# Kernel optimization log

Hardware: AMD Instinct MI355X
Metric: run time of the kernel (lower is better)

## Reference

```python
import jax, jax.numpy as jnp
import numpy as np

B, N, C = 64, 320, 768
H = 12
D = C // H  # 64 head dim


def setup_inputs() -> dict:
    key = jax.random.key(0)
    k1, k2, k3, k4, k5 = jax.random.split(key, 5)
    s = 0.02
    return {
        "x": jax.random.normal(k1, (B, N, C), jnp.float32),
        "w_qkv": jax.random.normal(k2, (3 * C, C), jnp.float32) * s,
        "b_qkv": jax.random.normal(k3, (3 * C,), jnp.float32) * s,
        "w_proj": jax.random.normal(k4, (C, C), jnp.float32) * s,
        "b_proj": jax.random.normal(k5, (C,), jnp.float32) * s,
        "num_t": 64,
        "num_s": 256,
    }


def reference(x, w_qkv, b_qkv, w_proj, b_proj, num_t, num_s):
    Bx, Nx, Cx = x.shape
    scale = 1.0 / jnp.sqrt(jnp.asarray(D, x.dtype))
    # qkv projection: [B,N,3C] -> [3,B,H,N,D]
    qkv = x @ w_qkv.T + b_qkv
    qkv = qkv.reshape(Bx, Nx, 3, H, D).transpose(2, 0, 3, 1, 4)
    q, k, v = qkv[0], qkv[1], qkv[2]
    q_t, q_s = q[:, :, :num_t], q[:, :, num_t:]
    k_t = k[:, :, :num_t]
    v_t = v[:, :, :num_t]
    # template self-attention: [B,H,num_t,num_t]
    attn_t = jax.nn.softmax(jnp.einsum("bhqd,bhkd->bhqk", q_t, k_t) * scale, axis=-1)
    x_t = jnp.einsum("bhqk,bhkd->bhqd", attn_t, v_t)
    x_t = x_t.transpose(0, 2, 1, 3).reshape(Bx, num_t, Cx)
    # search attends to all tokens: [B,H,num_s,N]
    attn_s = jax.nn.softmax(jnp.einsum("bhqd,bhkd->bhqk", q_s, k) * scale, axis=-1)
    x_s = jnp.einsum("bhqk,bhkd->bhqd", attn_s, v)
    x_s = x_s.transpose(0, 2, 1, 3).reshape(Bx, num_s, Cx)
    out = jnp.concatenate([x_t, x_s], axis=1)
    return out @ w_proj.T + b_proj
```

## Files before the change

### kernel.cpp

```cpp
#include <hip/hip_runtime.h>
#include <hip/hip_bf16.h>


typedef __attribute__((ext_vector_type(8))) short short8;
typedef __attribute__((ext_vector_type(4))) float f32x4;
typedef __hip_bfloat16 bf16;

#define NTOK 320
#define CDIM 768
#define NHEAD 12
#define MFMA16(a,b,c) __builtin_amdgcn_mfma_f32_16x16x32_bf16((a),(b),(c),0,0,0)

__device__ __forceinline__ unsigned short bfbits(float v) {
    bf16 h = __float2bfloat16(v);
    unsigned short u; __builtin_memcpy(&u, &h, 2);
    return u;
}

__device__ __forceinline__ short8 ldfrag(const bf16* p) { return *(const short8*)p; }
__device__ __forceinline__ short8 ldfrag(const float* p) {
    float4 a = *(const float4*)p;
    float4 b = *(const float4*)(p + 4);
    short8 r;
    r[0]=(short)bfbits(a.x); r[1]=(short)bfbits(a.y); r[2]=(short)bfbits(a.z); r[3]=(short)bfbits(a.w);
    r[4]=(short)bfbits(b.x); r[5]=(short)bfbits(b.y); r[6]=(short)bfbits(b.z); r[7]=(short)bfbits(b.w);
    return r;
}

__device__ __forceinline__ void stage16(const bf16* g, bf16* l) {
    __builtin_amdgcn_global_load_lds(
        (const __attribute__((address_space(1))) void*)g,
        (__attribute__((address_space(3))) void*)l, 16, 0, 0);
}

__global__ __launch_bounds__(256) void cvt_bf16_kernel(const float* __restrict__ src,
                                                       bf16* __restrict__ dst, int n8)
{
    int i = blockIdx.x * 256 + threadIdx.x;
    const int stride = gridDim.x * 256;
    for (; i < n8; i += stride) {
        const float4 a = ((const float4*)src)[2 * (size_t)i];
        const float4 b = ((const float4*)src)[2 * (size_t)i + 1];
        short8 r;
        r[0]=(short)bfbits(a.x); r[1]=(short)bfbits(a.y); r[2]=(short)bfbits(a.z); r[3]=(short)bfbits(a.w);
        r[4]=(short)bfbits(b.x); r[5]=(short)bfbits(b.y); r[6]=(short)bfbits(b.z); r[7]=(short)bfbits(b.w);
        ((short8*)dst)[i] = r;
    }
}

template<int NOUT, int EPI, int BF16B>
__global__ __launch_bounds__(256) void gemm_bt16(const bf16* __restrict__ A,
                                                 const void* __restrict__ Bmv,
                                                 const float* __restrict__ bias,
                                                 void* __restrict__ o0,
                                                 void* __restrict__ o1,
                                                 void* __restrict__ o2)
{
    __shared__ alignas(16) bf16 As[128 * 32];
    __shared__ alignas(16) bf16 Bs[128 * 32];
    const int tid  = threadIdx.x;
    const int lane = tid & 63;
    const int wv   = tid >> 6;
    const int r16  = lane & 15;
    const int kg   = lane >> 4;

    constexpr int GX  = NOUT / 128;
    constexpr int NWG = GX * 160;
    int flat = blockIdx.y * GX + blockIdx.x;
    flat = (flat & 7) * (NWG >> 3) + (flat >> 3);
    const int byy = flat / GX;
    const int bxx = flat - byy * GX;
    const int m0  = byy * 128;
    const int n0  = bxx * 128;
    const int wm  = (wv & 1) * 64;
    const int wn  = (wv >> 1) * 64;

    const bf16*  Ab   = A + (size_t)m0 * CDIM;
    const bf16*  Bb16 = (const bf16*)Bmv  + (size_t)n0 * CDIM;
    const float* Bb32 = (const float*)Bmv + (size_t)n0 * CDIM;

    const int ra0 = tid >> 2;
    const int ca0 = (tid & 3) * 8;

    bf16* lA0 = &As[(size_t)(wv * 64) * 8];
    bf16* lA1 = &As[(size_t)(wv * 64 + 256) * 8];
    bf16* lB0 = &Bs[(size_t)(wv * 64) * 8];
    bf16* lB1 = &Bs[(size_t)(wv * 64 + 256) * 8];

    f32x4 acc[4][4] = {};

    for (int k0 = 0; k0 < CDIM; k0 += 32) {
        if constexpr (BF16B) {
            __syncthreads();
            stage16(Ab   + (size_t)ra0        * CDIM + k0 + ca0, lA0);
            stage16(Ab   + (size_t)(ra0 + 64) * CDIM + k0 + ca0, lA1);
            stage16(Bb16 + (size_t)ra0        * CDIM + k0 + ca0, lB0);
            stage16(Bb16 + (size_t)(ra0 + 64) * CDIM + k0 + ca0, lB1);
            __syncthreads();
        } else {
            short8 gb0 = ldfrag(Bb32 + (size_t)ra0        * CDIM + k0 + ca0);
            short8 gb1 = ldfrag(Bb32 + (size_t)(ra0 + 64) * CDIM + k0 + ca0);
            __syncthreads();
            stage16(Ab + (size_t)ra0        * CDIM + k0 + ca0, lA0);
            stage16(Ab + (size_t)(ra0 + 64) * CDIM + k0 + ca0, lA1);
            *(short8*)&Bs[(size_t)tid * 8]         = gb0;
            *(short8*)&Bs[(size_t)(tid + 256) * 8] = gb1;
            __syncthreads();
        }

        short8 af[4], bfr[4];
        #pragma unroll
        for (int mt = 0; mt < 4; mt++)
            af[mt] = *(const short8*)&As[(wm + mt * 16 + r16) * 32 + kg * 8];
        #pragma unroll
        for (int nt = 0; nt < 4; nt++)
            bfr[nt] = *(const short8*)&Bs[(wn + nt * 16 + r16) * 32 + kg * 8];
        #pragma unroll
        for (int mt = 0; mt < 4; mt++)
            #pragma unroll
            for (int nt = 0; nt < 4; nt++)
                acc[mt][nt] = MFMA16(af[mt], bfr[nt], acc[mt][nt]);
    }

    #pragma unroll
    for (int nt = 0; nt < 4; nt++) {
        const int gn = n0 + wn + nt * 16 + r16;
        const float bv = bias[gn];
        if (EPI == 0) {
            const int which = gn / CDIM;
            const int rem   = gn - which * CDIM;
            const int hh    = rem >> 6;
            const int dd    = rem & 63;
            #pragma unroll
            for (int mt = 0; mt < 4; mt++) {
                const int gm0  = m0 + wm + mt * 16 + kg * 4;
                const int bidx = gm0 / NTOK;
                const int nn0  = gm0 - bidx * NTOK;
                float v[4];
                #pragma unroll
                for (int r = 0; r < 4; r++) v[r] = acc[mt][nt][r] + bv;
                if (which == 0) {
                    bf16* q = (bf16*)o0 + ((size_t)(bidx * NHEAD + hh) * NTOK + nn0) * 64 + dd;
                    #pragma unroll
                    for (int r = 0; r < 4; r++) q[(size_t)r * 64] = __float2bfloat16(v[r]);
                } else if (which == 1) {
                    bf16* k = (bf16*)o1 + ((size_t)(bidx * NHEAD + hh) * NTOK + nn0) * 64 + dd;
                    #pragma unroll
                    for (int r = 0; r < 4; r++) k[(size_t)r * 64] = __float2bfloat16(v[r]);
                } else {
                    ushort4 p;
                    unsigned short* ps = (unsigned short*)&p;
                    #pragma unroll
                    for (int r = 0; r < 4; r++) ps[r] = bfbits(v[r]);
                    *(ushort4*)((bf16*)o2 + ((size_t)(bidx * NHEAD + hh) * 64 + dd) * NTOK + nn0) = p;
                }
            }
        } else {
            float* out = (float*)o0;
            #pragma unroll
            for (int mt = 0; mt < 4; mt++) {
                const int gm0 = m0 + wm + mt * 16 + kg * 4;
                #pragma unroll
                for (int r = 0; r < 4; r++)
                    out[(size_t)(gm0 + r) * NOUT + gn] = acc[mt][nt][r] + bv;
            }
        }
    }
}

#define SW 324
__global__ __launch_bounds__(256) void attn_kernel(const bf16* __restrict__ q_ws,
                                                   const bf16* __restrict__ k_ws,
                                                   const bf16* __restrict__ vt_ws,
                                                   bf16* __restrict__ attn,
                                                   const int* __restrict__ numt_p)
{
    __shared__ alignas(16) float S[32 * SW];
    __shared__ float rowstat[32];
    int num_t = 64;
    if (numt_p) {
        int v = *numt_p;
        float f = __int_as_float(v);
        if (v >= 1 && v <= 319) num_t = v;
        else if (f >= 1.f && f <= 319.f) num_t = (int)f;
    }
    if (num_t <= 0 || num_t > NTOK || (num_t & 31)) num_t = 64;

    const int tid  = threadIdx.x;
    const int lane = tid & 63;
    const int w    = tid >> 6;
    const int r16  = lane & 15;
    const int kg   = lane >> 4;

    const int blk = blockIdx.x;
    const int bh  = blk / 10;
    const int qt  = blk - bh * 10;
    const int b   = bh / NHEAD;
    const int h   = bh - b * NHEAD;
    const int q0  = qt * 32;
    const int nk  = (q0 + 32 <= num_t) ? num_t : NTOK;
    const int nk16 = nk >> 4;

    const bf16* qp = q_ws  + (size_t)bh * NTOK * 64;
    const bf16* kp = k_ws  + (size_t)bh * NTOK * 64;
    const bf16* vp = vt_ws + (size_t)bh * 64 * NTOK;

    short8 qf[2][2];
    #pragma unroll
    for (int ks = 0; ks < 2; ks++)
        #pragma unroll
        for (int mt = 0; mt < 2; mt++)
            qf[ks][mt] = ldfrag(qp + (size_t)(q0 + mt * 16 + r16) * 64 + ks * 32 + kg * 8);

    const float scale = 0.125f;
    for (int nt = w; nt < nk16; nt += 4) {
        f32x4 a0 = {}, a1 = {};
        #pragma unroll
        for (int ks = 0; ks < 2; ks++) {
            short8 kf = ldfrag(kp + (size_t)(nt * 16 + r16) * 64 + ks * 32 + kg * 8);
            a0 = MFMA16(qf[ks][0], kf, a0);
            a1 = MFMA16(qf[ks][1], kf, a1);
        }
        #pragma unroll
        for (int r = 0; r < 4; r++) {
            S[(kg * 4 + r) * SW + nt * 16 + r16]      = a0[r] * scale;
            S[(16 + kg * 4 + r) * SW + nt * 16 + r16] = a1[r] * scale;
        }
    }
    __syncthreads();

    {
        const int row = tid >> 3;
        const int sub = tid & 7;
        float* Sr = S + row * SW;
        float mx = -1e30f;
        for (int c = sub * 4; c < nk; c += 32) {
            float4 t = *(float4*)&Sr[c];
            mx = fmaxf(mx, fmaxf(fmaxf(t.x, t.y), fmaxf(t.z, t.w)));
        }
        #pragma unroll
        for (int m = 1; m < 8; m <<= 1) mx = fmaxf(mx, __shfl_xor(mx, m));
        float sum = 0.f;
        for (int c = sub * 4; c < nk; c += 32) {
            float4 t = *(float4*)&Sr[c];
            t.x = __expf(t.x - mx); t.y = __expf(t.y - mx);
            t.z = __expf(t.z - mx); t.w = __expf(t.w - mx);
            sum += t.x + t.y + t.z + t.w;
            *(float4*)&Sr[c] = t;
        }
        #pragma unroll
        for (int m = 1; m < 8; m <<= 1) sum += __shfl_xor(sum, m);
        if (sub == 0) rowstat[row] = 1.0f / sum;
    }
    __syncthreads();

    const int mt  = w & 1;
    const int ntb = w >> 1;
    f32x4 o[2] = {};
    for (int ks = 0; ks < (nk >> 5); ks++) {
        const float* pr = &S[(mt * 16 + r16) * SW + ks * 32 + kg * 8];
        short8 af;
        #pragma unroll
        for (int j = 0; j < 8; j++) af[j] = (short)bfbits(pr[j]);
        #pragma unroll
        for (int i = 0; i < 2; i++) {
            const int nt = ntb + i * 2;
            short8 vf = ldfrag(vp + (size_t)(nt * 16 + r16) * NTOK + ks * 32 + kg * 8);
            o[i] = MFMA16(af, vf, o[i]);
        }
    }
    #pragma unroll
    for (int i = 0; i < 2; i++) {
        const int nt = ntb + i * 2;
        const int dd = nt * 16 + r16;
        #pragma unroll
        for (int r = 0; r < 4; r++) {
            const int qrow  = mt * 16 + kg * 4 + r;
            const float val = o[i][r] * rowstat[qrow];
            const int token = q0 + qrow;
            attn[(((size_t)b * NTOK + token) * NHEAD + h) * 64 + dd] = __float2bfloat16(val);
        }
    }
}

extern "C" void kernel_launch(void* const* d_in, const int* in_sizes, int n_in,
                              void* d_out, int out_size, void* d_ws, size_t ws_size,
                              hipStream_t stream)
{
    float* out = (float*)d_out;

    const float *x = nullptr, *w_qkv = nullptr, *b_qkv = nullptr,
                *w_proj = nullptr, *b_proj = nullptr;
    const int* numt_p = nullptr;
    for (int i = 0; i < n_in; i++) {
        switch (in_sizes[i]) {
            case 15728640: x      = (const float*)d_in[i]; break;
            case 1769472:  w_qkv  = (const float*)d_in[i]; break;
            case 2304:     b_qkv  = (const float*)d_in[i]; break;
            case 589824:   w_proj = (const float*)d_in[i]; break;
            case 768:      b_proj = (const float*)d_in[i]; break;
            case 1:        if (!numt_p) numt_p = (const int*)d_in[i]; break;
            default: break;
        }
    }
    if (!x || !w_qkv || !b_qkv || !w_proj || !b_proj) return;

    const size_t per      = (size_t)64 * NHEAD * NTOK * 64;
    const size_t wq_elems = (size_t)2304 * 768;
    const size_t wp_elems = (size_t)768 * 768;
    const size_t base_need = 4 * per * sizeof(bf16);
    const size_t full_need = base_need + (wq_elems + wp_elems) * sizeof(bf16);
    if (ws_size < base_need) return;
    const bool full = ws_size >= full_need;

    bf16* q_ws  = (bf16*)d_ws;
    bf16* k_ws  = q_ws  + per;
    bf16* vt_ws = k_ws  + per;
    bf16* attn  = vt_ws + per;
    bf16* x16   = attn;
    bf16* wq16  = attn + per;
    bf16* wp16  = wq16 + wq_elems;

    cvt_bf16_kernel<<<2048, 256, 0, stream>>>(x, x16, (int)(per / 8));
    if (full) {
        cvt_bf16_kernel<<<864, 256, 0, stream>>>(w_qkv, wq16, (int)(wq_elems / 8));
        cvt_bf16_kernel<<<288, 256, 0, stream>>>(w_proj, wp16, (int)(wp_elems / 8));
    }

    if (full)
        gemm_bt16<2304, 0, 1><<<dim3(18, 160), 256, 0, stream>>>(
            x16, wq16, b_qkv, q_ws, k_ws, vt_ws);
    else
        gemm_bt16<2304, 0, 0><<<dim3(18, 160), 256, 0, stream>>>(
            x16, w_qkv, b_qkv, q_ws, k_ws, vt_ws);

    attn_kernel<<<768 * 10, 256, 0, stream>>>(q_ws, k_ws, vt_ws, attn, numt_p);

    if (full)
        gemm_bt16<768, 1, 1><<<dim3(6, 160), 256, 0, stream>>>(
            attn, wp16, b_proj, out, nullptr, nullptr);
    else
        gemm_bt16<768, 1, 0><<<dim3(6, 160), 256, 0, stream>>>(
            attn, w_proj, b_proj, out, nullptr, nullptr);
}
```

Before: 398.8 us.

## Fuse bf16 conversion launches, remap attention blocks per XCD, store P as bf16

Merges the three fp32-to-bf16 conversion launches into one kernel that walks a concatenated index range, removing two launches. Remaps attention block IDs so that consecutive blocks sharing a batch-head land on the same XCD (blk&7 interleave), which should improve L2 reuse of K/V. After the softmax exp, probabilities are written in place as bf16, so the PV loop loads an MFMA fragment directly instead of converting eight floats per step. In-place aliasing of the bf16 rows inside the float rows relies on each row being handled only by its own threads before the barrier.

```diff
diff --git a/kernel.cpp b/kernel.cpp
--- a/kernel.cpp
+++ b/kernel.cpp
@@ -33,18 +33,24 @@
         (__attribute__((address_space(3))) void*)l, 16, 0, 0);
 }
 
-__global__ __launch_bounds__(256) void cvt_bf16_kernel(const float* __restrict__ src,
-                                                       bf16* __restrict__ dst, int n8)
+__global__ __launch_bounds__(256) void cvt3_kernel(const float* __restrict__ s0, bf16* __restrict__ d0, int n0,
+                                                   const float* __restrict__ s1, bf16* __restrict__ d1, int n1,
+                                                   const float* __restrict__ s2, bf16* __restrict__ d2, int n2)
 {
+    const int ntot = n0 + n1 + n2;
     int i = blockIdx.x * 256 + threadIdx.x;
     const int stride = gridDim.x * 256;
-    for (; i < n8; i += stride) {
-        const float4 a = ((const float4*)src)[2 * (size_t)i];
-        const float4 b = ((const float4*)src)[2 * (size_t)i + 1];
+    for (; i < ntot; i += stride) {
+        const float* s; bf16* d; int j = i;
+        if (j < n0)              { s = s0; d = d0; }
+        else if ((j -= n0) < n1) { s = s1; d = d1; }
+        else                     { j -= n1; s = s2; d = d2; }
+        const float4 a = ((const float4*)s)[2 * (size_t)j];
+        const float4 b = ((const float4*)s)[2 * (size_t)j + 1];
         short8 r;
         r[0]=(short)bfbits(a.x); r[1]=(short)bfbits(a.y); r[2]=(short)bfbits(a.z); r[3]=(short)bfbits(a.w);
         r[4]=(short)bfbits(b.x); r[5]=(short)bfbits(b.y); r[6]=(short)bfbits(b.z); r[7]=(short)bfbits(b.w);
-        ((short8*)dst)[i] = r;
+        ((short8*)d)[j] = r;
     }
 }
 
@@ -169,6 +175,7 @@
 }
 
 #define SW 324
+#define ATTN_NWG (768 * 10)
 __global__ __launch_bounds__(256) void attn_kernel(const bf16* __restrict__ q_ws,
                                                    const bf16* __restrict__ k_ws,
                                                    const bf16* __restrict__ vt_ws,
@@ -192,7 +199,8 @@
     const int r16  = lane & 15;
     const int kg   = lane >> 4;
 
-    const int blk = blockIdx.x;
+    int blk = blockIdx.x;
+    blk = (blk & 7) * (ATTN_NWG / 8) + (blk >> 3);
     const int bh  = blk / 10;
     const int qt  = blk - bh * 10;
     const int b   = bh / NHEAD;
@@ -233,6 +241,7 @@
         const int row = tid >> 3;
         const int sub = tid & 7;
         float* Sr = S + row * SW;
+        bf16*  Pr = (bf16*)Sr;
         float mx = -1e30f;
         for (int c = sub * 4; c < nk; c += 32) {
             float4 t = *(float4*)&Sr[c];
@@ -246,7 +255,9 @@
             t.x = __expf(t.x - mx); t.y = __expf(t.y - mx);
             t.z = __expf(t.z - mx); t.w = __expf(t.w - mx);
             sum += t.x + t.y + t.z + t.w;
-            *(float4*)&Sr[c] = t;
+            ushort4 p;
+            p.x = bfbits(t.x); p.y = bfbits(t.y); p.z = bfbits(t.z); p.w = bfbits(t.w);
+            *(ushort4*)&Pr[c] = p;
         }
         #pragma unroll
         for (int m = 1; m < 8; m <<= 1) sum += __shfl_xor(sum, m);
@@ -256,12 +267,10 @@
 
     const int mt  = w & 1;
     const int ntb = w >> 1;
+    const bf16* Pb = (const bf16*)S;
     f32x4 o[2] = {};
     for (int ks = 0; ks < (nk >> 5); ks++) {
-        const float* pr = &S[(mt * 16 + r16) * SW + ks * 32 + kg * 8];
-        short8 af;
-        #pragma unroll
-        for (int j = 0; j < 8; j++) af[j] = (short)bfbits(pr[j]);
+        short8 af = *(const short8*)&Pb[(size_t)(mt * 16 + r16) * (SW * 2) + ks * 32 + kg * 8];
         #pragma unroll
         for (int i = 0; i < 2; i++) {
             const int nt = ntb + i * 2;
@@ -321,11 +330,13 @@
     bf16* wq16  = attn + per;
     bf16* wp16  = wq16 + wq_elems;
 
-    cvt_bf16_kernel<<<2048, 256, 0, stream>>>(x, x16, (int)(per / 8));
-    if (full) {
-        cvt_bf16_kernel<<<864, 256, 0, stream>>>(w_qkv, wq16, (int)(wq_elems / 8));
-        cvt_bf16_kernel<<<288, 256, 0, stream>>>(w_proj, wp16, (int)(wp_elems / 8));
-    }
+    if (full)
+        cvt3_kernel<<<2048, 256, 0, stream>>>(x, x16, (int)(per / 8),
+                                              w_qkv, wq16, (int)(wq_elems / 8),
+                                              w_proj, wp16, (int)(wp_elems / 8));
+    else
+        cvt3_kernel<<<2048, 256, 0, stream>>>(x, x16, (int)(per / 8),
+                                              x, x16, 0, x, x16, 0);
 
     if (full)
         gemm_bt16<2304, 0, 1><<<dim3(18, 160), 256, 0, stream>>>(
@@ -334,7 +345,7 @@
         gemm_bt16<2304, 0, 0><<<dim3(18, 160), 256, 0, stream>>>(
             x16, w_qkv, b_qkv, q_ws, k_ws, vt_ws);
 
-    attn_kernel<<<768 * 10, 256, 0, stream>>>(q_ws, k_ws, vt_ws, attn, numt_p);
+    attn_kernel<<<ATTN_NWG, 256, 0, stream>>>(q_ws, k_ws, vt_ws, attn, numt_p);
 
     if (full)
         gemm_bt16<768, 1, 1><<<dim3(6, 160), 256, 0, stream>>>(
```

After: 389.8 us. 1.02x faster.
